# Performance work log

Measured on AMD Instinct MI355X. Metric: run time of the kernel, lower is better.

The kernel has to match this reference:

```python
import jax, jax.numpy as jnp
import numpy as np

SCORE_THRESH = 0.05
NMS_THRESH = 0.5
K = 1000            # max NMS candidates (fixed for jit; padded/masked)
IMG_W, IMG_H = 1333, 800


def setup_inputs() -> dict:
    key = jax.random.key(0)
    k1, k2, k3 = jax.random.split(key, 3)
    N, C = 200000, 81
    class_logits = jax.random.normal(k1, (N, C), dtype=jnp.float32) * 2.0
    # well-formed xyxy boxes inside the image
    cxcy = jax.random.uniform(k2, (N, 2), dtype=jnp.float32) * jnp.array([IMG_W, IMG_H], jnp.float32)
    wh = jax.random.uniform(k3, (N, 2), dtype=jnp.float32) * 200.0 + 1.0
    boxes = jnp.concatenate([cxcy - wh * 0.5, cxcy + wh * 0.5], axis=-1)
    return {"class_logits": class_logits, "boxes": boxes}


def _pairwise_iou(b):
    # b: [K, 4] xyxy -> [K, K]
    area = (b[:, 2] - b[:, 0]) * (b[:, 3] - b[:, 1])
    lt = jnp.maximum(b[:, None, :2], b[None, :, :2])
    rb = jnp.minimum(b[:, None, 2:], b[None, :, 2:])
    wh = jnp.clip(rb - lt, 0.0)
    inter = wh[..., 0] * wh[..., 1]
    return inter / (area[:, None] + area[None, :] - inter + 1e-9)


def reference(class_logits, boxes):
    N, C = class_logits.shape
    prob = jax.nn.softmax(class_logits, axis=-1)            # [N, C]
    # clip_to_image (TO_REMOVE=1 convention: clamp to size-1)
    bx = jnp.stack([
        jnp.clip(boxes[:, 0], 0.0, IMG_W - 1),
        jnp.clip(boxes[:, 1], 0.0, IMG_H - 1),
        jnp.clip(boxes[:, 2], 0.0, IMG_W - 1),
        jnp.clip(boxes[:, 3], 0.0, IMG_H - 1),
    ], axis=-1)                                             # [N, 4]
    flat = prob.reshape(-1)                                 # [N*C], class = idx % C
    idx = jnp.arange(N * C)
    valid = (flat > SCORE_THRESH) & (idx % C != 0)          # fg + score threshold
    masked = jnp.where(valid, flat, -jnp.inf)
    top_scores, top_idx = jax.lax.top_k(masked, K)          # sorted descending
    prop_idx = top_idx // C
    cls = top_idx % C
    bk = bx[prop_idx]                                       # [K, 4]
    valid_k = jnp.isfinite(top_scores)
    scores_k = jnp.where(valid_k, top_scores, 0.0)
    # class-aware greedy NMS over the (sorted) top-K candidates
    conflict = (_pairwise_iou(bk) > NMS_THRESH) & (cls[:, None] == cls[None, :])
    rng = jnp.arange(K)

    def body(i, keep):
        sup = jnp.any(keep & conflict[:, i] & (rng < i))
        return keep.at[i].set(keep[i] & ~sup)

    keep = jax.lax.fori_loop(0, K, body, valid_k)
    out = jnp.concatenate([bk, scores_k[:, None]], axis=-1) * keep[:, None].astype(bk.dtype)
    return out  # [K, 5]: (x1, y1, x2, y2, score), zeroed where suppressed/invalid
```

## Files before the change

### kernel.cpp

```cpp
#include <hip/hip_runtime.h>
#include <stdint.h>
#include <math.h>

#define N_CLS    81
#define TOPK     1000
#define LISTCAP  (1u << 21)
#define CAP2     16384
#define SCORE_TH 0.05f
#define IMG_W    1333.0f
#define IMG_H    800.0f
#define GH_REP   8

#define GH_BASE  1905

#define OFF_CNT    0
#define OFF_CNT2   8
#define OFF_GH     64
#define OFF_RH     4608
#define OFF_SORTED 8704
#define MEMSET_BYTES 16704
#define OFF_SEL    16768
#define OFF_SEL2   16793984
#define OFF_BOX    16925056
#define OFF_SCORE  16941056
#define OFF_CLS    16945056
#define OFF_MASK   16949056

typedef unsigned long long u64;

__global__ __launch_bounds__(256) void k_pass1(
        const float* __restrict__ logits, int nrows,
        u64* __restrict__ sel, unsigned* __restrict__ cnt,
        unsigned* __restrict__ ghist) {
    __shared__ unsigned lh[128];
    __shared__ u64 cbuf[2048];
    __shared__ unsigned lcnt, gbase;
    int tid = threadIdx.x, wv = tid >> 6, ln = tid & 63;
    for (int i = tid; i < 128; i += 256) lh[i] = 0;
    if (tid == 0) lcnt = 0;
    __syncthreads();

    int stride = gridDim.x * 16;
    for (int base = blockIdx.x * 16 + wv * 4; base < nrows; base += stride) {
        int nr = nrows - base; if (nr > 4) nr = 4;
        float v0[4], v1[4], m[4], e0[4], e1[4], s[4];
        #pragma unroll
        for (int k = 0; k < 4; k++) {
            bool ok = (k < nr);
            const float* rp = logits + (size_t)(ok ? base + k : base) * N_CLS;
            v0[k] = ok ? rp[ln] : 0.0f;
            v1[k] = (ok && ln < N_CLS - 64) ? rp[64 + ln] : -INFINITY;
        }
        #pragma unroll
        for (int k = 0; k < 4; k++) m[k] = fmaxf(v0[k], v1[k]);
        #pragma unroll
        for (int off = 32; off > 0; off >>= 1)
            #pragma unroll
            for (int k = 0; k < 4; k++) m[k] = fmaxf(m[k], __shfl_xor(m[k], off));
        #pragma unroll
        for (int k = 0; k < 4; k++) {
            e0[k] = expf(v0[k] - m[k]);
            e1[k] = (ln < N_CLS - 64) ? expf(v1[k] - m[k]) : 0.0f;
            s[k] = e0[k] + e1[k];
        }
        #pragma unroll
        for (int off = 32; off > 0; off >>= 1)
            #pragma unroll
            for (int k = 0; k < 4; k++) s[k] += __shfl_xor(s[k], off);

        #pragma unroll
        for (int k = 0; k < 4; k++) {
            if (k >= nr) break;
            float p0 = e0[k] / s[k];
            float p1 = e1[k] / s[k];
            bool c0 = (k < nr) && (ln != 0) && (p0 > SCORE_TH);
            bool c1 = (k < nr) && (ln < N_CLS - 64) && (p1 > SCORE_TH);
            unsigned fb0 = __float_as_uint(p0), fb1 = __float_as_uint(p1);
            if (c0) atomicAdd(&lh[(fb0 >> 19) - GH_BASE], 1u);
            if (c1) atomicAdd(&lh[(fb1 >> 19) - GH_BASE], 1u);
            u64 b0 = __ballot(c0), b1 = __ballot(c1);
            int n0 = __popcll(b0), n1 = __popcll(b1);
            if (n0 + n1 == 0) continue;
            unsigned wb = 0;
            if (ln == 0) wb = atomicAdd(&lcnt, (unsigned)(n0 + n1));
            wb = __shfl(wb, 0);
            u64 lt = (1ull << ln) - 1ull;
            unsigned flat = (unsigned)(base + k) * N_CLS + (unsigned)ln;
            if (c0) {
                unsigned pos = wb + (unsigned)__popcll(b0 & lt);
                u64 key = ((u64)fb0 << 32) | (u64)(0xFFFFFFu - flat);
                if (pos < 2048) cbuf[pos] = key;
                else { unsigned gp = atomicAdd(cnt, 1u); if (gp < LISTCAP) sel[gp] = key; }
            }
            if (c1) {
                unsigned pos = wb + (unsigned)n0 + (unsigned)__popcll(b1 & lt);
                u64 key = ((u64)fb1 << 32) | (u64)(0xFFFFFFu - (flat + 64u));
                if (pos < 2048) cbuf[pos] = key;
                else { unsigned gp = atomicAdd(cnt, 1u); if (gp < LISTCAP) sel[gp] = key; }
            }
        }
    }
    __syncthreads();
    unsigned* gh = ghist + (blockIdx.x & (GH_REP - 1)) * 128;
    for (int i = tid; i < 128; i += 256) {
        unsigned v = lh[i];
        if (v) atomicAdd(&gh[i], v);
    }
    unsigned total = lcnt; if (total > 2048u) total = 2048u;
    if (tid == 0) gbase = atomicAdd(cnt, total);
    __syncthreads();
    unsigned gb = gbase;
    for (unsigned i = tid; i < total; i += 256) {
        unsigned gp = gb + i;
        if (gp < LISTCAP) sel[gp] = cbuf[i];
    }
}

__device__ inline int scan_coarse(const unsigned* __restrict__ ghist, unsigned* c_above) {
    unsigned cum = 0;
    for (int i = 127; i >= 0; --i) {
        unsigned c = 0;
        #pragma unroll
        for (int r = 0; r < GH_REP; r++) c += ghist[r * 128 + i];
        if (cum + c >= TOPK) { *c_above = cum; return i; }
        cum += c;
    }
    *c_above = cum;
    return -1;
}

__global__ __launch_bounds__(256) void k_refine(
        const u64* __restrict__ sel, const unsigned* __restrict__ cnt,
        const unsigned* __restrict__ ghist, unsigned* __restrict__ rhist) {
    __shared__ unsigned lh[1024];
    __shared__ int sB;
    int tid = threadIdx.x;
    for (int i = tid; i < 1024; i += 256) lh[i] = 0;
    if (tid == 0) { unsigned ca; sB = scan_coarse(ghist, &ca); }
    __syncthreads();
    int B = sB;
    if (B < 0) return;
    unsigned Bbits = (unsigned)(B + GH_BASE);
    unsigned M = *cnt; if (M > LISTCAP) M = LISTCAP;
    unsigned stride = gridDim.x * blockDim.x;
    for (unsigned i = blockIdx.x * blockDim.x + tid; i < M; i += stride) {
        unsigned bits = (unsigned)(sel[i] >> 32);
        if ((bits >> 19) == Bbits) atomicAdd(&lh[(bits >> 9) & 1023u], 1u);
    }
    __syncthreads();
    for (int i = tid; i < 1024; i += 256) {
        unsigned v = lh[i];
        if (v) atomicAdd(&rhist[i], v);
    }
}

__global__ __launch_bounds__(256) void k_select(
        const u64* __restrict__ sel, const unsigned* __restrict__ cnt,
        const unsigned* __restrict__ ghist, const unsigned* __restrict__ rhist,
        u64* __restrict__ sel2, unsigned* __restrict__ cnt2) {
    __shared__ unsigned s4[256];
    __shared__ unsigned tbs;
    int tid = threadIdx.x, ln = tid & 63;
    unsigned ps = 0;
    #pragma unroll
    for (int k = 0; k < 4; k++) ps += rhist[tid * 4 + k];
    s4[tid] = ps;
    __syncthreads();
    if (tid == 0) {
        unsigned c_above;
        int B = scan_coarse(ghist, &c_above);
        unsigned tb = 0;
        if (B >= 0) {
            unsigned cab = c_above;
            int g = -1;
            for (int i = 255; i >= 0; --i) {
                if (cab + s4[i] >= TOPK) { g = i; break; }
                cab += s4[i];
            }
            int sb = 0;
            if (g >= 0) {
                for (int i = g * 4 + 3; i >= g * 4; --i) {
                    unsigned c = rhist[i];
                    if (cab + c >= TOPK) { sb = i; break; }
                    cab += c;
                }
            }
            tb = ((unsigned)(B + GH_BASE) << 19) | ((unsigned)sb << 9);
        }
        tbs = tb;
    }
    __syncthreads();
    unsigned tb = tbs;
    unsigned M = *cnt; if (M > LISTCAP) M = LISTCAP;
    unsigned stride = gridDim.x * blockDim.x;
    for (unsigned ibase = blockIdx.x * blockDim.x; ibase < M; ibase += stride) {
        unsigned i = ibase + tid;
        bool act = (i < M);
        u64 key = act ? sel[i] : 0ull;
        bool c = act && ((unsigned)(key >> 32) >= tb);
        u64 b = __ballot(c);
        int n = __popcll(b);
        if (n == 0) continue;
        unsigned wb = 0;
        if (ln == 0) wb = atomicAdd(cnt2, (unsigned)n);
        wb = __shfl(wb, 0);
        if (c) {
            unsigned pos = wb + (unsigned)__popcll(b & ((1ull << ln) - 1ull));
            if (pos < CAP2) sel2[pos] = key;
        }
    }
}

__global__ __launch_bounds__(256) void k_rank(
        const u64* __restrict__ sel2, const unsigned* __restrict__ cnt2,
        u64* __restrict__ sorted) {
    __shared__ u64 ch[2048];
    unsigned S = *cnt2; if (S > CAP2) S = CAP2;
    if (blockIdx.x * 256u >= S) return;
    unsigned t = blockIdx.x * 256u + threadIdx.x;
    u64 my = (t < S) ? sel2[t] : 0ull;
    int r = 0;
    for (unsigned c0 = 0; c0 < S; c0 += 2048) {
        unsigned n = S - c0; if (n > 2048) n = 2048;
        __syncthreads();
        for (unsigned i = threadIdx.x; i < n; i += 256) ch[i] = sel2[c0 + i];
        __syncthreads();
        if (t < S)
            for (unsigned j = 0; j < n; j++) r += (ch[j] > my) ? 1 : 0;
    }
    if (t < S && r < TOPK) sorted[r] = my;
}

__global__ __launch_bounds__(256) void k_decode(
        const u64* __restrict__ sorted, const float* __restrict__ boxes,
        float* __restrict__ boxK, float* __restrict__ scoreK, int* __restrict__ clsK) {
    int t = blockIdx.x * blockDim.x + threadIdx.x;
    if (t >= TOPK) return;
    u64 key = sorted[t];
    if (key != 0ull) {
        float sc = __uint_as_float((unsigned)(key >> 32));
        unsigned fi = 0xFFFFFFu - (unsigned)(key & 0xFFFFFFFFull);
        unsigned prop = fi / N_CLS;
        int cls = (int)(fi - prop * N_CLS);
        const float* b = boxes + (size_t)prop * 4;
        boxK[t * 4 + 0] = fminf(fmaxf(b[0], 0.0f), IMG_W - 1.0f);
        boxK[t * 4 + 1] = fminf(fmaxf(b[1], 0.0f), IMG_H - 1.0f);
        boxK[t * 4 + 2] = fminf(fmaxf(b[2], 0.0f), IMG_W - 1.0f);
        boxK[t * 4 + 3] = fminf(fmaxf(b[3], 0.0f), IMG_H - 1.0f);
        scoreK[t] = sc;
        clsK[t] = cls;
    } else {
        boxK[t * 4 + 0] = 0.0f; boxK[t * 4 + 1] = 0.0f;
        boxK[t * 4 + 2] = 0.0f; boxK[t * 4 + 3] = 0.0f;
        scoreK[t] = 0.0f;
        clsK[t] = -1;
    }
}

__global__ __launch_bounds__(256) void k_conflict(
        const float* __restrict__ boxK, const int* __restrict__ clsK,
        u64* __restrict__ mask) {
    int t = blockIdx.x * blockDim.x + threadIdx.x;
    if (t >= TOPK * 16) return;
    int i = t >> 4, w = t & 15;
    float x1 = boxK[i * 4 + 0], y1 = boxK[i * 4 + 1];
    float x2 = boxK[i * 4 + 2], y2 = boxK[i * 4 + 3];
    int ci = clsK[i];
    float ai = (x2 - x1) * (y2 - y1);
    u64 m = 0;
    int jbase = w << 6;
    for (int jj = 0; jj < 64; jj++) {
        int j = jbase + jj;
        if (j >= TOPK) break;
        float u1 = boxK[j * 4 + 0], w1 = boxK[j * 4 + 1];
        float u2 = boxK[j * 4 + 2], w2 = boxK[j * 4 + 3];
        float aj = (u2 - u1) * (w2 - w1);
        float ww = fmaxf(fminf(x2, u2) - fmaxf(x1, u1), 0.0f);
        float hh = fmaxf(fminf(y2, w2) - fmaxf(y1, w1), 0.0f);
        float inter = ww * hh;
        float iou = inter / (ai + aj - inter + 1e-9f);
        if (iou > 0.5f && ci == clsK[j]) m |= (1ull << jj);
    }
    mask[(size_t)i * 16 + w] = m;
}

__global__ __launch_bounds__(1024) void k_nms_out(
        const u64* __restrict__ mask, const float* __restrict__ boxK,
        const float* __restrict__ scoreK, float* __restrict__ out) {
    __shared__ u64 words[16];
    __shared__ int changed;
    int tid = threadIdx.x, wv = tid >> 6, ln = tid & 63;
    bool valid = (tid < TOPK) && (scoreK[tid] > 0.0f);
    u64 row[16];
    #pragma unroll
    for (int w = 0; w < 16; w++)
        row[w] = (tid < TOPK) ? mask[(size_t)tid * 16 + w] : 0ull;
    u64 lowmask = (1ull << ln) - 1ull;
    bool keep = valid;
    for (int it = 0; it < 1024; ++it) {
        u64 b = __ballot(keep);
        if (ln == 0) words[wv] = b;
        if (tid == 0) changed = 0;
        __syncthreads();
        u64 sup = 0;
        for (int w = 0; w <= wv; w++) {
            u64 kw = words[w];
            if (w == wv) kw &= lowmask;
            sup |= row[w] & kw;
        }
        bool nk = valid && (sup == 0ull);
        if (nk != keep) changed = 1;
        keep = nk;
        __syncthreads();
        if (!changed) break;
    }
    if (tid < TOPK) {
        float x1 = boxK[tid * 4 + 0], y1 = boxK[tid * 4 + 1];
        float x2 = boxK[tid * 4 + 2], y2 = boxK[tid * 4 + 3];
        float sc = scoreK[tid];
        out[tid * 5 + 0] = keep ? x1 : 0.0f;
        out[tid * 5 + 1] = keep ? y1 : 0.0f;
        out[tid * 5 + 2] = keep ? x2 : 0.0f;
        out[tid * 5 + 3] = keep ? y2 : 0.0f;
        out[tid * 5 + 4] = keep ? sc : 0.0f;
    }
}

extern "C" void kernel_launch(void* const* d_in, const int* in_sizes, int n_in,
                              void* d_out, int out_size, void* d_ws, size_t ws_size,
                              hipStream_t stream) {
    const float* logits = (const float*)d_in[0];
    const float* boxes  = (const float*)d_in[1];
    float* out = (float*)d_out;
    int nrows = in_sizes[0] / N_CLS;

    char* w = (char*)d_ws;
    unsigned* cnt    = (unsigned*)(w + OFF_CNT);
    unsigned* cnt2   = (unsigned*)(w + OFF_CNT2);
    unsigned* ghist  = (unsigned*)(w + OFF_GH);
    unsigned* rhist  = (unsigned*)(w + OFF_RH);
    u64* sorted      = (u64*)(w + OFF_SORTED);
    u64* sel         = (u64*)(w + OFF_SEL);
    u64* sel2        = (u64*)(w + OFF_SEL2);
    float* boxK      = (float*)(w + OFF_BOX);
    float* scoreK    = (float*)(w + OFF_SCORE);
    int* clsK        = (int*)(w + OFF_CLS);
    u64* mask        = (u64*)(w + OFF_MASK);

    hipMemsetAsync(w, 0, MEMSET_BYTES, stream);

    k_pass1<<<1024, 256, 0, stream>>>(logits, nrows, sel, cnt, ghist);
    k_refine<<<256, 256, 0, stream>>>(sel, cnt, ghist, rhist);
    k_select<<<256, 256, 0, stream>>>(sel, cnt, ghist, rhist, sel2, cnt2);
    k_rank<<<CAP2 / 256, 256, 0, stream>>>(sel2, cnt2, sorted);
    k_decode<<<(TOPK + 255) / 256, 256, 0, stream>>>(sorted, boxes, boxK, scoreK, clsK);
    k_conflict<<<(TOPK * 16 + 255) / 256, 256, 0, stream>>>(boxK, clsK, mask);
    k_nms_out<<<1, 1024, 0, stream>>>(mask, boxK, scoreK, out);
}
```

Baseline: 213.1 us.

## Map one softmax row per thread with logit-space threshold prefilter in pass1

Rewrites the first pass so each thread owns a full row instead of a wavefront cooperatively processing four rows. Max and sum are computed serially per thread, the sum using a pairwise-tree stack for accuracy. Candidates are then prefiltered in logit space against m+log(0.049*s) before any exp or divide. This removes the cross-lane shuffles and ballots but leaves each thread reading a row at stride 81 floats, so global loads are uncoalesced. The launch grid now scales with row count.

```diff
diff --git a/kernel.cpp b/kernel.cpp
--- a/kernel.cpp
+++ b/kernel.cpp
@@ -35,68 +35,61 @@
     __shared__ unsigned lh[128];
     __shared__ u64 cbuf[2048];
     __shared__ unsigned lcnt, gbase;
-    int tid = threadIdx.x, wv = tid >> 6, ln = tid & 63;
+    int tid = threadIdx.x;
     for (int i = tid; i < 128; i += 256) lh[i] = 0;
     if (tid == 0) lcnt = 0;
     __syncthreads();
 
-    int stride = gridDim.x * 16;
-    for (int base = blockIdx.x * 16 + wv * 4; base < nrows; base += stride) {
-        int nr = nrows - base; if (nr > 4) nr = 4;
-        float v0[4], v1[4], m[4], e0[4], e1[4], s[4];
+    int row = blockIdx.x * 256 + tid;
+    if (row < nrows) {
+        const float* rp = logits + (size_t)row * N_CLS;
+
+        float m0 = rp[0], m1 = rp[1], m2 = rp[2], m3 = rp[3];
+        for (int j = 4; j + 3 < N_CLS; j += 4) {
+            m0 = fmaxf(m0, rp[j]);
+            m1 = fmaxf(m1, rp[j + 1]);
+            m2 = fmaxf(m2, rp[j + 2]);
+            m3 = fmaxf(m3, rp[j + 3]);
+        }
+        m0 = fmaxf(m0, rp[N_CLS - 1]);
+        float m = fmaxf(fmaxf(m0, m1), fmaxf(m2, m3));
+
+        float stk0 = 0.f, stk1 = 0.f, stk2 = 0.f, stk3 = 0.f, stk4 = 0.f, stk5 = 0.f;
+        float s = 0.f;
         #pragma unroll
-        for (int k = 0; k < 4; k++) {
-            bool ok = (k < nr);
-            const float* rp = logits + (size_t)(ok ? base + k : base) * N_CLS;
-            v0[k] = ok ? rp[ln] : 0.0f;
-            v1[k] = (ok && ln < N_CLS - 64) ? rp[64 + ln] : -INFINITY;
-        }
-        #pragma unroll
-        for (int k = 0; k < 4; k++) m[k] = fmaxf(v0[k], v1[k]);
-        #pragma unroll
-        for (int off = 32; off > 0; off >>= 1)
-            #pragma unroll
-            for (int k = 0; k < 4; k++) m[k] = fmaxf(m[k], __shfl_xor(m[k], off));
-        #pragma unroll
-        for (int k = 0; k < 4; k++) {
-            e0[k] = expf(v0[k] - m[k]);
-            e1[k] = (ln < N_CLS - 64) ? expf(v1[k] - m[k]) : 0.0f;
-            s[k] = e0[k] + e1[k];
-        }
-        #pragma unroll
-        for (int off = 32; off > 0; off >>= 1)
-            #pragma unroll
-            for (int k = 0; k < 4; k++) s[k] += __shfl_xor(s[k], off);
-
-        #pragma unroll
-        for (int k = 0; k < 4; k++) {
-            if (k >= nr) break;
-            float p0 = e0[k] / s[k];
-            float p1 = e1[k] / s[k];
-            bool c0 = (k < nr) && (ln != 0) && (p0 > SCORE_TH);
-            bool c1 = (k < nr) && (ln < N_CLS - 64) && (p1 > SCORE_TH);
-            unsigned fb0 = __float_as_uint(p0), fb1 = __float_as_uint(p1);
-            if (c0) atomicAdd(&lh[(fb0 >> 19) - GH_BASE], 1u);
-            if (c1) atomicAdd(&lh[(fb1 >> 19) - GH_BASE], 1u);
-            u64 b0 = __ballot(c0), b1 = __ballot(c1);
-            int n0 = __popcll(b0), n1 = __popcll(b1);
-            if (n0 + n1 == 0) continue;
-            unsigned wb = 0;
-            if (ln == 0) wb = atomicAdd(&lcnt, (unsigned)(n0 + n1));
-            wb = __shfl(wb, 0);
-            u64 lt = (1ull << ln) - 1ull;
-            unsigned flat = (unsigned)(base + k) * N_CLS + (unsigned)ln;
-            if (c0) {
-                unsigned pos = wb + (unsigned)__popcll(b0 & lt);
-                u64 key = ((u64)fb0 << 32) | (u64)(0xFFFFFFu - flat);
-                if (pos < 2048) cbuf[pos] = key;
-                else { unsigned gp = atomicAdd(cnt, 1u); if (gp < LISTCAP) sel[gp] = key; }
-            }
-            if (c1) {
-                unsigned pos = wb + (unsigned)n0 + (unsigned)__popcll(b1 & lt);
-                u64 key = ((u64)fb1 << 32) | (u64)(0xFFFFFFu - (flat + 64u));
-                if (pos < 2048) cbuf[pos] = key;
-                else { unsigned gp = atomicAdd(cnt, 1u); if (gp < LISTCAP) sel[gp] = key; }
+        for (int i = 0; i < 64; i++) {
+            const int l = ((i & 1) << 5) | ((i & 2) << 3) | ((i & 4) << 1) |
+                          ((i & 8) >> 1) | ((i & 16) >> 3) | ((i & 32) >> 5);
+            float x = expf(rp[l] - m);
+            if (l < 17) x += expf(rp[l + 64] - m);
+            if (i & 1) { x = stk0 + x;
+              if (i & 2) { x = stk1 + x;
+                if (i & 4) { x = stk2 + x;
+                  if (i & 8) { x = stk3 + x;
+                    if (i & 16) { x = stk4 + x;
+                      if (i & 32) { s = stk5 + x; } else stk5 = x;
+                    } else stk4 = x;
+                  } else stk3 = x;
+                } else stk2 = x;
+              } else stk1 = x;
+            } else stk0 = x;
+        }
+
+        float thr = m + logf(0.049f * s);
+        unsigned rbase = (unsigned)row * N_CLS;
+        for (int j = 1; j < N_CLS; j++) {
+            float v = rp[j];
+            if (v > thr) {
+                float e = expf(v - m);
+                float p = e / s;
+                if (p > SCORE_TH) {
+                    unsigned fb = __float_as_uint(p);
+                    atomicAdd(&lh[(fb >> 19) - GH_BASE], 1u);
+                    u64 key = ((u64)fb << 32) | (u64)(0xFFFFFFu - (rbase + (unsigned)j));
+                    unsigned pos = atomicAdd(&lcnt, 1u);
+                    if (pos < 2048) cbuf[pos] = key;
+                    else { unsigned gp = atomicAdd(cnt, 1u); if (gp < LISTCAP) sel[gp] = key; }
+                }
             }
         }
     }
@@ -349,7 +342,8 @@
 
     hipMemsetAsync(w, 0, MEMSET_BYTES, stream);
 
-    k_pass1<<<1024, 256, 0, stream>>>(logits, nrows, sel, cnt, ghist);
+    int nblk = (nrows + 255) / 256;
+    k_pass1<<<nblk, 256, 0, stream>>>(logits, nrows, sel, cnt, ghist);
     k_refine<<<256, 256, 0, stream>>>(sel, cnt, ghist, rhist);
     k_select<<<256, 256, 0, stream>>>(sel, cnt, ghist, rhist, sel2, cnt2);
     k_rank<<<CAP2 / 256, 256, 0, stream>>>(sel2, cnt2, sorted);
```

Result: slower. 273.0 us (+28.1%).
